# Optimization experiments

Hardware: AMD Instinct MI355X
Metric: run time of the kernel (lower is better)

The kernel has to match this reference:

```python
import jax, jax.numpy as jnp
import numpy as np

N = 100000
E = 3200000
IN_DIM = 256
HID = 128
HID2 = 64
K = 16


def setup_inputs() -> dict:
    key = jax.random.key(0)
    ks = jax.random.split(key, 12)
    x = jax.random.normal(ks[0], (N, IN_DIM), dtype=jnp.float32)
    edge_index = jax.random.randint(ks[1], (2, E), 0, N, dtype=jnp.int64)
    edge_weight = jax.random.uniform(ks[2], (E,), dtype=jnp.float32)
    s = lambda f: 1.0 / np.sqrt(f)
    W0 = jax.random.normal(ks[3], (IN_DIM, HID), dtype=jnp.float32) * s(IN_DIM)
    b0 = jnp.zeros((HID,), jnp.float32)
    P0w = jax.random.normal(ks[4], (IN_DIM, HID), dtype=jnp.float32) * s(IN_DIM)
    P0b = jnp.zeros((HID,), jnp.float32)
    W1 = jax.random.normal(ks[5], (HID, HID2), dtype=jnp.float32) * s(HID)
    b1 = jnp.zeros((HID2,), jnp.float32)
    P1w = jax.random.normal(ks[6], (HID, HID2), dtype=jnp.float32) * s(HID)
    P1b = jnp.zeros((HID2,), jnp.float32)
    W2 = jax.random.normal(ks[7], (HID2, K), dtype=jnp.float32) * s(HID2)
    b2 = jnp.zeros((K,), jnp.float32)
    return {"x": x, "edge_index": edge_index, "edge_weight": edge_weight,
            "W0": W0, "b0": b0, "P0w": P0w, "P0b": P0b,
            "W1": W1, "b1": b1, "P1w": P1w, "P1b": P1b,
            "W2": W2, "b2": b2}


def _gcn_norm(edge_index, edge_weight, n):
    # add self loops (weight 1), symmetric normalization per PyG gcn_norm
    loop = jnp.arange(n, dtype=edge_index.dtype)
    row = jnp.concatenate([edge_index[0], loop])
    col = jnp.concatenate([edge_index[1], loop])
    w = jnp.concatenate([edge_weight, jnp.ones((n,), edge_weight.dtype)])
    deg = jax.ops.segment_sum(w, col, num_segments=n)
    dinv = jnp.where(deg > 0, jax.lax.rsqrt(deg), 0.0)
    return row, col, dinv[row] * w * dinv[col]


def reference(x, edge_index, edge_weight, W0, b0, P0w, P0b, W1, b1, P1w, P1b, W2, b2):
    n = x.shape[0]
    row, col, nw = _gcn_norm(edge_index, edge_weight, n)

    def gcn(h, W, b):
        hW = h @ W  # transform first (PyG GCNConv), then scatter-aggregate
        agg = jax.ops.segment_sum(nw[:, None] * hW[row], col, num_segments=n)
        return agg + b

    # layer 0: skip is Linear(input_dim, hidden); dropout = identity (eval)
    h = jax.nn.selu(gcn(x, W0, b0) + (x @ P0w + P0b))
    # layer 1: skip is Linear(hidden, hidden//2)
    h = jax.nn.selu(gcn(h, W1, b1) + (h @ P1w + P1b))
    # layer 2: no skip, no dropout
    h = jax.nn.selu(gcn(h, W2, b2))
    return jax.nn.softmax(h, axis=-1)
```

## Files before the change

### kernel.cpp

```cpp
#include <hip/hip_runtime.h>
#include <hip/hip_fp16.h>
#include <cmath>

#define IN_DIM 256
#define HID 128
#define HID2 64
#define NODES_PB 256
#define NBKT_MAX 448
#define BCAP 9216
#define CHB 3328
#define CH 4096
#define SMEM_BIN (4 * NBKT_MAX * 4 + CHB * 9)

struct __align__(8) EdgeP { int s; float w; };
union H4 { __half h[4]; uint2 u; };
union H2 { __half2 h2; uint u; };

using f16x8 = __attribute__((ext_vector_type(8))) _Float16;
using f32x4 = __attribute__((ext_vector_type(4))) float;

__device__ __forceinline__ float selu_f(float x) {
    const float scale = 1.0507009873554805f;
    const float alpha = 1.6732632423543772f;
    return x > 0.f ? scale * x : scale * alpha * expm1f(x);
}


__global__ void zero_ints(int* p, int n) {
    int i = blockIdx.x * blockDim.x + threadIdx.x;
    if (i < n) p[i] = 0;
}

__global__ void transpose_w(const float* __restrict__ B1, const float* __restrict__ B2,
                            __half* __restrict__ WT, int K, int C1, int C2) {
    int c = blockIdx.x;
    for (int k = threadIdx.x; k < K; k += blockDim.x) {
        float v = (c < C1) ? B1[(size_t)k * C1 + c] : B2[(size_t)k * C2 + (c - C1)];
        WT[(size_t)c * K + k] = __float2half(v);
    }
}

__global__ void deg_dinv(const EdgeP* __restrict__ ell, int* cnt, float* dinv, int n, int cap) {
    int wid = (blockIdx.x * blockDim.x + threadIdx.x) >> 6;
    int lane = threadIdx.x & 63;
    if (wid >= n) return;
    size_t base = (size_t)wid * cap;
    int len = min(cnt[wid], cap);
    float s = 0.f;
    for (int i = lane; i < len; i += 64) s += ell[base + i].w;
#pragma unroll
    for (int o = 32; o; o >>= 1) s += __shfl_xor(s, o);
    if (lane == 0) {
        dinv[wid] = rsqrtf(s + 1.0f);
        cnt[wid] = len;
    }
}

template <int PER>
__device__ __forceinline__ void wave0_excl_scan(const int* lds_in, int* lds_out, int nb, int tid) {
    if (tid < 64) {
        int r[PER];
        int sum = 0;
#pragma unroll
        for (int k = 0; k < PER; ++k) {
            int idx = tid * PER + k;
            int v = (idx < nb) ? lds_in[idx] : 0;
            r[k] = sum;
            sum += v;
        }
        int run = sum;
#pragma unroll
        for (int o = 1; o < 64; o <<= 1) {
            int t = __shfl_up(run, o);
            if (tid >= o) run += t;
        }
        int excl = run - sum;
#pragma unroll
        for (int k = 0; k < PER; ++k) {
            int idx = tid * PER + k;
            if (idx < nb) lds_out[idx] = excl + r[k];
        }
    }
}

__global__ __launch_bounds__(256) void bin_gemm0(
    const float* __restrict__ A, const __half* __restrict__ WT,
    const float* __restrict__ bias1, const float* __restrict__ bias2,
    __half* __restrict__ outA, __half* __restrict__ outB, int M,
    const int* __restrict__ ei, const float* __restrict__ ew,
    int* cnt_or_bcur, EdgeP* __restrict__ dst_buf,
    int E, int cap, int epb, int sblocks, int nb, int mode) {
    const int tid = threadIdx.x;
    __shared__ __align__(16) char smem[SMEM_BIN];

    if ((int)blockIdx.x < sblocks) {
        int lo = blockIdx.x * epb;
        int hi = min(E, lo + epb);
        if (mode == 1) {
            int* gwcur = (int*)smem;
            int* chist = gwcur + NBKT_MAX;
            int* coff = chist + NBKT_MAX;
            int* ccur = coff + NBKT_MAX;
            int* sortedS = ccur + NBKT_MAX;
            float* sortedW = (float*)(sortedS + CHB);
            unsigned char* smap = (unsigned char*)(sortedW + CHB);

            if (hi - lo <= CHB) {
                int cn = hi - lo;
                for (int i = tid; i < nb; i += 256) chist[i] = 0;
                __syncthreads();
                for (int r0 = 0; r0 < cn; r0 += 2048) {
                    int d[8];
#pragma unroll
                    for (int j = 0; j < 8; ++j) {
                        int r = r0 + j * 256 + tid;
                        d[j] = (r < cn) ? ei[E + lo + r] : -1;
                    }
#pragma unroll
                    for (int j = 0; j < 8; ++j)
                        if (d[j] >= 0) atomicAdd(&chist[d[j] >> 8], 1);
                }
                __syncthreads();
                wave0_excl_scan<7>(chist, coff, nb, tid);
                __syncthreads();
                for (int b = tid; b < nb; b += 256) {
                    int h = chist[b];
                    gwcur[b] = h ? atomicAdd(&cnt_or_bcur[b], h) : 0;
                    ccur[b] = coff[b];
                }
                __syncthreads();
                for (int r0 = 0; r0 < cn; r0 += 2048) {
                    int d[8], s8[8];
                    float w8[8];
#pragma unroll
                    for (int j = 0; j < 8; ++j) {
                        int r = r0 + j * 256 + tid;
                        d[j] = -1;
                        if (r < cn) {
                            int e = lo + r;
                            d[j] = ei[E + e];
                            s8[j] = ei[e];
                            w8[j] = ew[e];
                        }
                    }
#pragma unroll
                    for (int j = 0; j < 8; ++j)
                        if (d[j] >= 0) {
                            int b = d[j] >> 8;
                            int slot = atomicAdd(&ccur[b], 1);
                            sortedS[slot] = (s8[j] << 8) | (d[j] & 255) | ((b >> 8) << 25);
                            sortedW[slot] = w8[j];
                            smap[slot] = (unsigned char)(b & 255);
                        }
                }
                __syncthreads();
                for (int i0 = 0; i0 < cn; i0 += 2048) {
                    int key[8], bb[8];
                    float wv[8];
#pragma unroll
                    for (int j = 0; j < 8; ++j) {
                        int i = i0 + j * 256 + tid;
                        bb[j] = -1;
                        if (i < cn) {
                            key[j] = sortedS[i];
                            wv[j] = sortedW[i];
                            bb[j] = smap[i] | (((key[j] >> 25) & 1) << 8);
                        }
                    }
#pragma unroll
                    for (int j = 0; j < 8; ++j)
                        if (bb[j] >= 0) {
                            int i = i0 + j * 256 + tid;
                            int addr = gwcur[bb[j]] + (i - coff[bb[j]]);
                            if (addr < BCAP) {
                                EdgeP p; p.s = key[j] & 0x01FFFFFF; p.w = wv[j];
                                dst_buf[(size_t)bb[j] * BCAP + addr] = p;
                            }
                        }
                }
            } else {
                for (int i = tid; i < nb; i += 256) chist[i] = 0;
                __syncthreads();
                for (int e0 = lo; e0 < hi; e0 += 2048) {
                    int d[8];
#pragma unroll
                    for (int j = 0; j < 8; ++j) {
                        int e = e0 + j * 256 + tid;
                        d[j] = (e < hi) ? ei[E + e] : -1;
                    }
#pragma unroll
                    for (int j = 0; j < 8; ++j)
                        if (d[j] >= 0) atomicAdd(&chist[d[j] >> 8], 1);
                }
                __syncthreads();
                for (int b = tid; b < nb; b += 256) {
                    int h = chist[b];
                    gwcur[b] = h ? atomicAdd(&cnt_or_bcur[b], h) : 0;
                }
                __syncthreads();
                for (int c0 = lo; c0 < hi; c0 += CHB) {
                    int cn = min(CHB, hi - c0);
                    for (int i = tid; i < nb; i += 256) chist[i] = 0;
                    __syncthreads();
                    for (int r0 = 0; r0 < cn; r0 += 2048) {
                        int d[8];
#pragma unroll
                        for (int j = 0; j < 8; ++j) {
                            int r = r0 + j * 256 + tid;
                            d[j] = (r < cn) ? ei[E + c0 + r] : -1;
                        }
#pragma unroll
                        for (int j = 0; j < 8; ++j)
                            if (d[j] >= 0) atomicAdd(&chist[d[j] >> 8], 1);
                    }
                    __syncthreads();
                    wave0_excl_scan<7>(chist, coff, nb, tid);
                    __syncthreads();
                    for (int b = tid; b < nb; b += 256) ccur[b] = coff[b];
                    __syncthreads();
                    for (int r0 = 0; r0 < cn; r0 += 2048) {
                        int d[8], s8[8];
                        float w8[8];
#pragma unroll
                        for (int j = 0; j < 8; ++j) {
                            int r = r0 + j * 256 + tid;
                            d[j] = -1;
                            if (r < cn) {
                                int e = c0 + r;
                                d[j] = ei[E + e];
                                s8[j] = ei[e];
                                w8[j] = ew[e];
                            }
                        }
#pragma unroll
                        for (int j = 0; j < 8; ++j)
                            if (d[j] >= 0) {
                                int b = d[j] >> 8;
                                int slot = atomicAdd(&ccur[b], 1);
                                sortedS[slot] = (s8[j] << 8) | (d[j] & 255) | ((b >> 8) << 25);
                                sortedW[slot] = w8[j];
                                smap[slot] = (unsigned char)(b & 255);
                            }
                    }
                    __syncthreads();
                    for (int i0 = 0; i0 < cn; i0 += 2048) {
                        int key[8], bb[8];
                        float wv[8];
#pragma unroll
                        for (int j = 0; j < 8; ++j) {
                            int i = i0 + j * 256 + tid;
                            bb[j] = -1;
                            if (i < cn) {
                                key[j] = sortedS[i];
                                wv[j] = sortedW[i];
                                bb[j] = smap[i] | (((key[j] >> 25) & 1) << 8);
                            }
                        }
#pragma unroll
                        for (int j = 0; j < 8; ++j)
                            if (bb[j] >= 0) {
                                int i = i0 + j * 256 + tid;
                                int addr = gwcur[bb[j]] + (i - coff[bb[j]]);
                                if (addr < BCAP) {
                                    EdgeP p; p.s = key[j] & 0x01FFFFFF; p.w = wv[j];
                                    dst_buf[(size_t)bb[j] * BCAP + addr] = p;
                                }
                            }
                    }
                    __syncthreads();
                    for (int b = tid; b < nb; b += 256) gwcur[b] += chist[b];
                    __syncthreads();
                }
            }
        } else {
            for (int base = lo; base < hi; base += 2048) {
                int r[8], c[8], pos[8];
                float wv[8];
#pragma unroll
                for (int j = 0; j < 8; ++j) {
                    int e = base + j * 256 + tid;
                    c[j] = -1;
                    if (e < hi) { r[j] = ei[e]; c[j] = ei[E + e]; wv[j] = ew[e]; }
                }
#pragma unroll
                for (int j = 0; j < 8; ++j)
                    if (c[j] >= 0) pos[j] = atomicAdd(&cnt_or_bcur[c[j]], 1);
#pragma unroll
                for (int j = 0; j < 8; ++j)
                    if (c[j] >= 0 && pos[j] < cap) {
                        EdgeP p; p.s = r[j]; p.w = wv[j];
                        dst_buf[(size_t)c[j] * cap + pos[j]] = p;
                    }
            }
        }
        return;
    }

    __half* sA16 = (__half*)smem;
    __half* sB16 = (__half*)(smem + 10240);
    const int bid = blockIdx.x - sblocks;
    const int mi = ((bid >> 4) << 3) + (bid & 7);
    const int m0 = mi * 128;
    const int n0 = ((bid >> 3) & 1) * 128;
    if (m0 >= M) return;
    const int lane = tid & 63;
    const int wv = tid >> 6;
    const int wr = (wv >> 1) * 64;
    const int wc = (wv & 1) * 64;
    const int lr = lane & 15, lk = lane >> 4;

    f32x4 zero = {0.f, 0.f, 0.f, 0.f};
    f32x4 acc[4][4];
#pragma unroll
    for (int i = 0; i < 4; ++i)
#pragma unroll
        for (int j = 0; j < 4; ++j) acc[i][j] = zero;

    for (int k0 = 0; k0 < IN_DIM; k0 += 32) {
#pragma unroll
        for (int p = 0; p < 4; ++p) {
            int f4 = p * 256 + tid;
            int r = f4 >> 3;
            int kk = (f4 & 7) << 2;
            int row = m0 + r;
            float4 v = make_float4(0.f, 0.f, 0.f, 0.f);
            if (row < M) v = *(const float4*)(A + (size_t)row * IN_DIM + k0 + kk);
            H4 h;
            h.h[0] = __float2half(v.x); h.h[1] = __float2half(v.y);
            h.h[2] = __float2half(v.z); h.h[3] = __float2half(v.w);
            *(uint2*)&sA16[r * 40 + kk] = h.u;
        }
#pragma unroll
        for (int p = 0; p < 2; ++p) {
            int f = p * 256 + tid;
            int c = f >> 2;
            int kc = (f & 3) << 3;
            *(uint4*)&sB16[c * 40 + kc] =
                *(const uint4*)(WT + (size_t)(n0 + c) * IN_DIM + k0 + kc);
        }
        __syncthreads();
        f16x8 af[4], bf[4];
#pragma unroll
        for (int i = 0; i < 4; ++i)
            af[i] = *(const f16x8*)&sA16[(wr + i * 16 + lr) * 40 + lk * 8];
#pragma unroll
        for (int j = 0; j < 4; ++j)
            bf[j] = *(const f16x8*)&sB16[(wc + j * 16 + lr) * 40 + lk * 8];
#pragma unroll
        for (int i = 0; i < 4; ++i)
#pragma unroll
            for (int j = 0; j < 4; ++j)
                acc[i][j] = __builtin_amdgcn_mfma_f32_16x16x32_f16(af[i], bf[j], acc[i][j], 0, 0, 0);
        __syncthreads();
    }

#pragma unroll
    for (int i = 0; i < 4; ++i) {
        int rowb = m0 + wr + i * 16 + lk * 4;
#pragma unroll
        for (int j = 0; j < 4; ++j) {
            int col = wc + j * 16 + lr;
#pragma unroll
            for (int r = 0; r < 4; ++r) {
                int row = rowb + r;
                if (row < M) {
                    if (n0 == 0)
                        outA[(size_t)row * HID + col] = __float2half(acc[i][j][r]);
                    else
                        outB[(size_t)row * HID + col] =
                            __float2half(acc[i][j][r] + bias1[col] + bias2[col]);
                }
            }
        }
    }
}

__global__ __launch_bounds__(256) void bucket_build(
    const EdgeP* __restrict__ recs, const int* __restrict__ bcur,
    EdgeP* __restrict__ ell, int* __restrict__ cnt, float* __restrict__ dinv,
    int n, int cap) {
    __shared__ int lcnt[NODES_PB];
    __shared__ float ldeg[NODES_PB];
    __shared__ int chist[NODES_PB];
    __shared__ int coff[NODES_PB];
    __shared__ int ccur[NODES_PB];
    __shared__ __align__(8) int sortedS[CH];
    __shared__ float sortedW[CH];
    __shared__ unsigned char cmap[CH];
    int b = blockIdx.x, tid = threadIdx.x;
    lcnt[tid] = 0;
    ldeg[tid] = 0.f;
    __syncthreads();
    int m = min(bcur[b], BCAP);
    const EdgeP* rbase = recs + (size_t)b * BCAP;
    for (int c0 = 0; c0 < m; c0 += CH) {
        int cn = min(CH, m - c0);
        chist[tid] = 0;
        __syncthreads();
        for (int i0 = 0; i0 < cn; i0 += 2048) {
            EdgeP p[8];
            int ok[8];
#pragma unroll
            for (int j = 0; j < 8; ++j) {
                int i = i0 + j * 256 + tid;
                ok[j] = (i < cn);
                if (ok[j]) p[j] = rbase[c0 + i];
            }
#pragma unroll
            for (int j = 0; j < 8; ++j)
                if (ok[j]) {
                    int dl = p[j].s & 255;
                    atomicAdd(&chist[dl], 1);
                    atomicAdd(&ldeg[dl], p[j].w);
                }
        }
        __syncthreads();
        wave0_excl_scan<4>(chist, coff, NODES_PB, tid);
        __syncthreads();
        ccur[tid] = coff[tid];
        __syncthreads();
        for (int i0 = 0; i0 < cn; i0 += 2048) {
            EdgeP p[8];
            int ok[8];
#pragma unroll
            for (int j = 0; j < 8; ++j) {
                int i = i0 + j * 256 + tid;
                ok[j] = (i < cn);
                if (ok[j]) p[j] = rbase[c0 + i];
            }
#pragma unroll
            for (int j = 0; j < 8; ++j)
                if (ok[j]) {
                    int dl = p[j].s & 255;
                    int slot = atomicAdd(&ccur[dl], 1);
                    sortedS[slot] = p[j].s >> 8;
                    sortedW[slot] = p[j].w;
                    cmap[slot] = (unsigned char)dl;
                }
        }
        __syncthreads();
        for (int i0 = 0; i0 < cn; i0 += 2048) {
            int s8[8], dl8[8];
            float w8[8];
#pragma unroll
            for (int j = 0; j < 8; ++j) {
                int i = i0 + j * 256 + tid;
                dl8[j] = -1;
                if (i < cn) {
                    s8[j] = sortedS[i];
                    w8[j] = sortedW[i];
                    dl8[j] = cmap[i];
                }
            }
#pragma unroll
            for (int j = 0; j < 8; ++j)
                if (dl8[j] >= 0) {
                    int i = i0 + j * 256 + tid;
                    int rank = lcnt[dl8[j]] + (i - coff[dl8[j]]);
                    if (rank < cap) {
                        EdgeP q; q.s = s8[j]; q.w = w8[j];
                        ell[((size_t)(b * NODES_PB + dl8[j])) * cap + rank] = q;
                    }
                }
        }
        __syncthreads();
        lcnt[tid] += chist[tid];
        __syncthreads();
    }
    int v = b * NODES_PB + tid;
    if (v < n) {
        cnt[v] = min(lcnt[tid], cap);
        dinv[v] = rsqrtf(ldeg[tid] + 1.0f);
    }
}

__global__ __launch_bounds__(256) void gemm1_fused(
    const __half* __restrict__ A, const __half* __restrict__ WT,
    const float* __restrict__ bias1, const float* __restrict__ bias2,
    __half* __restrict__ outA, __half* __restrict__ outB, int M) {
    const int tid = threadIdx.x;
    __shared__ __align__(16) __half sA16[128 * 40];
    __shared__ __align__(16) __half sB16[128 * 40];
    const int m0 = blockIdx.x * 128;
    const int lane = tid & 63;
    const int wv = tid >> 6;
    const int wr = (wv >> 1) * 64;
    const int wc = (wv & 1) * 64;
    const int lr = lane & 15, lk = lane >> 4;

    f32x4 zero = {0.f, 0.f, 0.f, 0.f};
    f32x4 acc[4][4];
#pragma unroll
    for (int i = 0; i < 4; ++i)
#pragma unroll
        for (int j = 0; j < 4; ++j) acc[i][j] = zero;

    for (int k0 = 0; k0 < HID; k0 += 32) {
#pragma unroll
        for (int p = 0; p < 2; ++p) {
            int f = p * 256 + tid;
            int r = f >> 2;
            int kc = (f & 3) << 3;
            int row = m0 + r;
            uint4 v = make_uint4(0, 0, 0, 0);
            if (row < M) v = *(const uint4*)(A + (size_t)row * HID + k0 + kc);
            *(uint4*)&sA16[r * 40 + kc] = v;
        }
#pragma unroll
        for (int p = 0; p < 2; ++p) {
            int f = p * 256 + tid;
            int c = f >> 2;
            int kc = (f & 3) << 3;
            *(uint4*)&sB16[c * 40 + kc] =
                *(const uint4*)(WT + (size_t)c * HID + k0 + kc);
        }
        __syncthreads();
        f16x8 af[4], bf[4];
#pragma unroll
        for (int i = 0; i < 4; ++i)
            af[i] = *(const f16x8*)&sA16[(wr + i * 16 + lr) * 40 + lk * 8];
#pragma unroll
        for (int j = 0; j < 4; ++j)
            bf[j] = *(const f16x8*)&sB16[(wc + j * 16 + lr) * 40 + lk * 8];
#pragma unroll
        for (int i = 0; i < 4; ++i)
#pragma unroll
            for (int j = 0; j < 4; ++j)
                acc[i][j] = __builtin_amdgcn_mfma_f32_16x16x32_f16(af[i], bf[j], acc[i][j], 0, 0, 0);
        __syncthreads();
    }

#pragma unroll
    for (int i = 0; i < 4; ++i) {
        int rowb = m0 + wr + i * 16 + lk * 4;
#pragma unroll
        for (int j = 0; j < 4; ++j) {
            int col = wc + j * 16 + lr;
#pragma unroll
            for (int r = 0; r < 4; ++r) {
                int row = rowb + r;
                if (row < M) {
                    if (wc == 0)
                        outA[(size_t)row * HID2 + col] = __float2half(acc[i][j][r]);
                    else {
                        int c = col - HID2;
                        outB[(size_t)row * HID2 + c] =
                            __float2half(acc[i][j][r] + bias1[c] + bias2[c]);
                    }
                }
            }
        }
    }
}

__global__ __launch_bounds__(256) void aggregate128(
    const __half* __restrict__ hW, __half* __restrict__ S,
    const float* __restrict__ dinv, const int* __restrict__ cnt,
    const EdgeP* __restrict__ ell, int cap, int n) {
    int v = (blockIdx.x * 256 + threadIdx.x) >> 6;
    int lane = threadIdx.x & 63;
    if (v >= n) return;
    float di = dinv[v];
    H2 svh; svh.u = *(const uint*)&S[(size_t)v * HID + lane * 2];
    float2 sv = __half22float2(svh.h2);
    H2 selfh; selfh.u = *(const uint*)&hW[(size_t)v * HID + lane * 2];
    float2 selff = __half22float2(selfh.h2);
    float selfx = sv.x + di * di * selff.x;
    float selfy = sv.y + di * di * selff.y;

    size_t base = (size_t)v * cap;
    int len = cnt[v];
    float ax[4] = {0.f, 0.f, 0.f, 0.f};
    float ay[4] = {0.f, 0.f, 0.f, 0.f};
    int i = 0;
    for (; i + 8 <= len; i += 8) {
        EdgeP p[8];
        float dv[8];
        uint h[8];
#pragma unroll
        for (int j = 0; j < 8; ++j) p[j] = ell[base + i + j];
#pragma unroll
        for (int j = 0; j < 8; ++j) {
            dv[j] = dinv[p[j].s];
            h[j] = *(const uint*)&hW[(size_t)p[j].s * HID + lane * 2];
        }
#pragma unroll
        for (int j = 0; j < 8; ++j) {
            float t = dv[j] * p[j].w;
            H2 hh; hh.u = h[j];
            float2 hf = __half22float2(hh.h2);
            ax[j & 3] = fmaf(t, hf.x, ax[j & 3]);
            ay[j & 3] = fmaf(t, hf.y, ay[j & 3]);
        }
    }
    for (; i < len; ++i) {
        EdgeP p = ell[base + i];
        float t = dinv[p.s] * p.w;
        H2 hh; hh.u = *(const uint*)&hW[(size_t)p.s * HID + lane * 2];
        float2 hf = __half22float2(hh.h2);
        ax[0] = fmaf(t, hf.x, ax[0]);
        ay[0] = fmaf(t, hf.y, ay[0]);
    }
    float sx = selfx + di * ((ax[0] + ax[1]) + (ax[2] + ax[3]));
    float sy = selfy + di * ((ay[0] + ay[1]) + (ay[2] + ay[3]));
    H2 o;
    o.h2.x = __float2half(selu_f(sx));
    o.h2.y = __float2half(selu_f(sy));
    *(uint*)&S[(size_t)v * HID + lane * 2] = o.u;
}

__global__ __launch_bounds__(256) void agg64_gemm2(
    const __half* __restrict__ hW, const __half* __restrict__ S,
    const float* __restrict__ dinv, const int* __restrict__ cnt,
    const EdgeP* __restrict__ ell, int cap,
    const float* __restrict__ W2, __half* __restrict__ out16, int n) {
    __shared__ float sW[64 * 16];
    __shared__ float sh[4][64];
    int tid = threadIdx.x;
#pragma unroll
    for (int i = 0; i < 4; ++i) sW[i * 256 + tid] = W2[i * 256 + tid];

    int g = tid >> 6, f = tid & 63;
    int v = blockIdx.x * 4 + g;
    if (v < n) {
        float di = dinv[v];
        float self = __half2float(S[(size_t)v * 64 + f]) +
                     di * di * __half2float(hW[(size_t)v * 64 + f]);
        size_t base = (size_t)v * cap;
        int len = cnt[v];
        float a[4] = {0.f, 0.f, 0.f, 0.f};
        int i = 0;
        for (; i + 8 <= len; i += 8) {
            EdgeP p[8];
            float dv[8];
            __half hv[8];
#pragma unroll
            for (int j = 0; j < 8; ++j) p[j] = ell[base + i + j];
#pragma unroll
            for (int j = 0; j < 8; ++j) {
                dv[j] = dinv[p[j].s];
                hv[j] = hW[(size_t)p[j].s * 64 + f];
            }
#pragma unroll
            for (int j = 0; j < 8; ++j)
                a[j & 3] = fmaf(dv[j] * p[j].w, __half2float(hv[j]), a[j & 3]);
        }
        for (; i < len; ++i) {
            EdgeP p = ell[base + i];
            a[0] = fmaf(dinv[p.s] * p.w, __half2float(hW[(size_t)p.s * 64 + f]), a[0]);
        }
        sh[g][f] = selu_f(self + di * ((a[0] + a[1]) + (a[2] + a[3])));
    }
    __syncthreads();
    if (v < n && f < 16) {
        float acc = 0.f;
#pragma unroll
        for (int k = 0; k < 64; ++k) acc = fmaf(sh[g][k], sW[k * 16 + f], acc);
        out16[(size_t)v * 16 + f] = __float2half(acc);
    }
}

__global__ __launch_bounds__(256) void agg_softmax(
    const __half* __restrict__ hW, const float* __restrict__ b2,
    const float* __restrict__ dinv, const int* __restrict__ cnt,
    const EdgeP* __restrict__ ell, int cap,
    float* __restrict__ out, int n) {
    int tid = threadIdx.x;
    int g = tid >> 4, f = tid & 15;
    int v = blockIdx.x * 16 + g;
    if (v >= n) return;
    float di = dinv[v];
    float acc = b2[f] + di * di * __half2float(hW[(size_t)v * 16 + f]);
    size_t base = (size_t)v * cap;
    int len = cnt[v];
    float a[4] = {0.f, 0.f, 0.f, 0.f};
    int i = 0;
    for (; i + 4 <= len; i += 4) {
        EdgeP p[4];
        float dv[4];
        __half hv[4];
#pragma unroll
        for (int j = 0; j < 4; ++j) p[j] = ell[base + i + j];
#pragma unroll
        for (int j = 0; j < 4; ++j) {
            dv[j] = dinv[p[j].s];
            hv[j] = hW[(size_t)p[j].s * 16 + f];
        }
#pragma unroll
        for (int j = 0; j < 4; ++j)
            a[j] = fmaf(dv[j] * p[j].w, __half2float(hv[j]), a[j]);
    }
    for (; i < len; ++i) {
        EdgeP p = ell[base + i];
        a[0] = fmaf(dinv[p.s] * p.w, __half2float(hW[(size_t)p.s * 16 + f]), a[0]);
    }
    acc += di * ((a[0] + a[1]) + (a[2] + a[3]));
    acc = selu_f(acc);
    float m = acc;
    m = fmaxf(m, __shfl_xor(m, 1));
    m = fmaxf(m, __shfl_xor(m, 2));
    m = fmaxf(m, __shfl_xor(m, 4));
    m = fmaxf(m, __shfl_xor(m, 8));
    float ex = expf(acc - m);
    float sm = ex;
    sm += __shfl_xor(sm, 1);
    sm += __shfl_xor(sm, 2);
    sm += __shfl_xor(sm, 4);
    sm += __shfl_xor(sm, 8);
    out[(size_t)v * 16 + f] = ex / sm;
}

extern "C" void kernel_launch(void* const* d_in, const int* in_sizes, int n_in,
                              void* d_out, int out_size, void* d_ws, size_t ws_size,
                              hipStream_t stream) {
    const float* x = (const float*)d_in[0];
    const int* ei = (const int*)d_in[1];
    const float* ew = (const float*)d_in[2];
    const float* W0 = (const float*)d_in[3];
    const float* b0 = (const float*)d_in[4];
    const float* P0w = (const float*)d_in[5];
    const float* P0b = (const float*)d_in[6];
    const float* W1 = (const float*)d_in[7];
    const float* b1 = (const float*)d_in[8];
    const float* P1w = (const float*)d_in[9];
    const float* P1b = (const float*)d_in[10];
    const float* W2 = (const float*)d_in[11];
    const float* b2 = (const float*)d_in[12];
    float* out = (float*)d_out;
    const int n = in_sizes[0] / IN_DIM;
    const int E = in_sizes[2];
    const int NB = (n + NODES_PB - 1) / NODES_PB;

    auto al = [](size_t b) { return (b + 255) & ~(size_t)255; };
    size_t oCnt = 0;
    size_t oDinv = oCnt + al((size_t)n * 4);
    size_t oBcur = oDinv + al((size_t)n * 4);
    size_t oWT0 = oBcur + al((size_t)NBKT_MAX * 4);
    size_t oWT1 = oWT0 + al((size_t)IN_DIM * (HID * 2) * 2);
    size_t oA = oWT1 + al((size_t)HID * HID * 2);
    size_t oB = oA + al((size_t)n * HID * 2);
    size_t oEll = oB + al((size_t)n * HID * 2);
    size_t szEll96 = al((size_t)n * 96 * 8);
    size_t szEll80 = al((size_t)n * 80 * 8);
    size_t szRec = al((size_t)NB * BCAP * 8);
    size_t szCD = al((size_t)n * HID2 * 2) + al((size_t)n * 16 * 2);
    size_t szR = szRec > szCD ? szRec : szCD;

    int cap;
    int mode;
    if (NB <= NBKT_MAX && oEll + szEll96 + szR <= ws_size) { cap = 96; mode = 1; }
    else if (oEll + szEll96 + szCD <= ws_size) { cap = 96; mode = 0; }
    else { cap = 80; mode = 0; }

    char* base = (char*)d_ws;
    int* cnt = (int*)(base + oCnt);
    float* dinv = (float*)(base + oDinv);
    int* bcur = (int*)(base + oBcur);
    __half* WT0 = (__half*)(base + oWT0);
    __half* WT1 = (__half*)(base + oWT1);
    __half* bufA = (__half*)(base + oA);
    __half* bufB = (__half*)(base + oB);
    EdgeP* ell = (EdgeP*)(base + oEll);
    size_t oR = oEll + (cap == 96 ? szEll96 : szEll80);
    EdgeP* recs = (EdgeP*)(base + oR);
    __half* bufC = (__half*)(base + oR);
    __half* bufD = (__half*)(base + oR + al((size_t)n * HID2 * 2));

    int gx = (n + 127) / 128;
    int gxp = (gx + 7) & ~7;
    int gemmBlocks = gxp * 2;
    int SBn = (E + CHB - 1) / CHB;
    if (SBn < 256) SBn = 256;
    int epb = (E + SBn - 1) / SBn;

    transpose_w<<<2 * HID, 128, 0, stream>>>(W0, P0w, WT0, IN_DIM, HID, HID);
    transpose_w<<<HID, 128, 0, stream>>>(W1, P1w, WT1, HID, HID2, HID2);

    if (mode == 1) {
        zero_ints<<<(NBKT_MAX + 255) / 256, 256, 0, stream>>>(bcur, NBKT_MAX);
        bin_gemm0<<<SBn + gemmBlocks, 256, 0, stream>>>(
            x, WT0, b0, P0b, bufA, bufB, n, ei, ew, bcur, recs,
            E, cap, epb, SBn, NB, 1);
        bucket_build<<<NB, NODES_PB, 0, stream>>>(recs, bcur, ell, cnt, dinv, n, cap);
    } else {
        zero_ints<<<(n + 255) / 256, 256, 0, stream>>>(cnt, n);
        bin_gemm0<<<SBn + gemmBlocks, 256, 0, stream>>>(
            x, WT0, b0, P0b, bufA, bufB, n, ei, ew, cnt, ell,
            E, cap, epb, SBn, NB, 0);
        int nbW = (n * 64 + 255) / 256;
        deg_dinv<<<nbW, 256, 0, stream>>>(ell, cnt, dinv, n, cap);
    }

    aggregate128<<<(n * 64 + 255) / 256, 256, 0, stream>>>(bufA, bufB, dinv, cnt, ell, cap, n);

    gemm1_fused<<<gx, 256, 0, stream>>>(bufB, WT1, b1, P1b, bufA, bufC, n);

    agg64_gemm2<<<(n + 3) / 4, 256, 0, stream>>>(bufA, bufC, dinv, cnt, ell, cap, W2, bufD, n);
    agg_softmax<<<(n + 15) / 16, 256, 0, stream>>>(bufD, b2, dinv, cnt, ell, cap, out, n);
}
```

Baseline: 502.3 us.

## Register-prefetch next K tile in fused GEMM and shrink bin chunk size

The x@W GEMM loop now preloads the next 32-wide K slice of A and W^T into registers while the current slice sits in shared memory. This hides global-load latency behind the MFMA work. It also lowers the CHB binning chunk constant, which shrinks the shared memory used by the binning blocks and may raise occupancy. The cost is extra registers per thread for the prefetch buffers, plus more binning chunks to process.

```diff
diff --git a/kernel.cpp b/kernel.cpp
--- a/kernel.cpp
+++ b/kernel.cpp
@@ -8,7 +8,7 @@
 #define NODES_PB 256
 #define NBKT_MAX 448
 #define BCAP 9216
-#define CHB 3328
+#define CHB 2048
 #define CH 4096
 #define SMEM_BIN (4 * NBKT_MAX * 4 + CHB * 9)
 
@@ -309,6 +309,11 @@
     const int wc = (wv & 1) * 64;
     const int lr = lane & 15, lk = lane >> 4;
 
+    const int ar = tid >> 3;
+    const int ak = (tid & 7) << 2;
+    const int bc = tid >> 2;
+    const int bk = (tid & 3) << 3;
+
     f32x4 zero = {0.f, 0.f, 0.f, 0.f};
     f32x4 acc[4][4];
 #pragma unroll
@@ -316,27 +321,39 @@
 #pragma unroll
         for (int j = 0; j < 4; ++j) acc[i][j] = zero;
 
+    float4 aReg[4];
+    uint4 bReg[2];
+#pragma unroll
+    for (int p = 0; p < 4; ++p) {
+        int row = m0 + ar + p * 32;
+        aReg[p] = (row < M) ? *(const float4*)(A + (size_t)row * IN_DIM + ak)
+                            : make_float4(0.f, 0.f, 0.f, 0.f);
+    }
+#pragma unroll
+    for (int p = 0; p < 2; ++p)
+        bReg[p] = *(const uint4*)(WT + (size_t)(n0 + bc + p * 64) * IN_DIM + bk);
+
     for (int k0 = 0; k0 < IN_DIM; k0 += 32) {
 #pragma unroll
         for (int p = 0; p < 4; ++p) {
-            int f4 = p * 256 + tid;
-            int r = f4 >> 3;
-            int kk = (f4 & 7) << 2;
-            int row = m0 + r;
-            float4 v = make_float4(0.f, 0.f, 0.f, 0.f);
-            if (row < M) v = *(const float4*)(A + (size_t)row * IN_DIM + k0 + kk);
             H4 h;
-            h.h[0] = __float2half(v.x); h.h[1] = __float2half(v.y);
-            h.h[2] = __float2half(v.z); h.h[3] = __float2half(v.w);
-            *(uint2*)&sA16[r * 40 + kk] = h.u;
-        }
-#pragma unroll
-        for (int p = 0; p < 2; ++p) {
-            int f = p * 256 + tid;
-            int c = f >> 2;
-            int kc = (f & 3) << 3;
-            *(uint4*)&sB16[c * 40 + kc] =
-                *(const uint4*)(WT + (size_t)(n0 + c) * IN_DIM + k0 + kc);
+            h.h[0] = __float2half(aReg[p].x); h.h[1] = __float2half(aReg[p].y);
+            h.h[2] = __float2half(aReg[p].z); h.h[3] = __float2half(aReg[p].w);
+            *(uint2*)&sA16[(ar + p * 32) * 40 + ak] = h.u;
+        }
+#pragma unroll
+        for (int p = 0; p < 2; ++p)
+            *(uint4*)&sB16[(bc + p * 64) * 40 + bk] = bReg[p];
+        if (k0 + 32 < IN_DIM) {
+#pragma unroll
+            for (int p = 0; p < 4; ++p) {
+                int row = m0 + ar + p * 32;
+                aReg[p] = (row < M) ? *(const float4*)(A + (size_t)row * IN_DIM + k0 + 32 + ak)
+                                    : make_float4(0.f, 0.f, 0.f, 0.f);
+            }
+#pragma unroll
+            for (int p = 0; p < 2; ++p)
+                bReg[p] = *(const uint4*)(WT + (size_t)(n0 + bc + p * 64) * IN_DIM + k0 + 32 + bk);
         }
         __syncthreads();
         f16x8 af[4], bf[4];
```

Result: no change. 506.2 us (+0.8%).
